# Optimization experiments

Hardware: AMD Instinct MI355X
Metric: run time of the kernel (lower is better)

The kernel has to match this reference:

```python
import jax, jax.numpy as jnp
import numpy as np

B, N, E, S, HOPS, OD = 32, 325, 64, 12, 3, 1


def setup_inputs() -> dict:
    key = jax.random.key(0)
    ks = jax.random.split(key, 16)
    rn = lambda k, sh: jax.random.normal(k, sh, dtype=jnp.float32)
    return {
        "hidden": rn(ks[0], (B, N, E)),
        "supports": jax.random.uniform(ks[1], (2, N, N), dtype=jnp.float32),
        "target": rn(ks[2], (B, S, N, OD)),
        "memory": rn(ks[3], (HOPS + 1, B, N, E)),
        "nodevec1": rn(ks[4], (N, E)),
        "nodevec2": rn(ks[5], (N, E)),
        "gru_w_ih": rn(ks[6], (3 * E, OD)) * 0.1,
        "gru_w_hh": rn(ks[7], (3 * E, E)) * 0.1,
        "gru_b_ih": rn(ks[8], (3 * E,)) * 0.1,
        "gru_b_hh": rn(ks[9], (3 * E,)) * 0.1,
        "sent_w": rn(ks[10], (HOPS, E, E)) * 0.1,  # sentinel Linear (no bias), stored pre-transposed
        "bn_gamma": jnp.ones((HOPS, N), dtype=jnp.float32),
        "bn_beta": jnp.zeros((HOPS, N), dtype=jnp.float32),
        "gconv_w": rn(ks[11], (HOPS, 7 * E, E)) * 0.05,  # order*support_len+1 = 7 chunks
        "gconv_b": rn(ks[12], (HOPS, E)) * 0.05,
        "out_w": rn(ks[13], (E, OD)) * 0.1,
        "out_b": rn(ks[14], (OD,)) * 0.1,
    }


def _bn(x, gamma, beta, eps=1e-5):
    # nn.BatchNorm1d(num_nodes) on (B, N, E): channel dim is N, stats over (B, E) (training-mode batch stats)
    mean = x.mean(axis=(0, 2), keepdims=True)
    var = x.var(axis=(0, 2), keepdims=True)
    return (x - mean) / jnp.sqrt(var + eps) * gamma[None, :, None] + beta[None, :, None]


def _gconv(x, sup_list, score, W, b):
    # order=2, support_len=3 -> 1 + 2*3 = 7 concatenated chunks, then Linear(7E -> E)
    outs = [x]
    for adj in sup_list:
        x1 = jnp.einsum('nm,bme->bne', adj, x)
        outs.append(jnp.einsum('bnm,bme->bne', score, x1))
        x2 = jnp.einsum('nm,bme->bne', adj, x1)
        outs.append(jnp.einsum('bnm,bme->bne', score, x2))
    return jnp.concatenate(outs, axis=-1) @ W + b


def reference(hidden, supports, target, memory, nodevec1, nodevec2,
              gru_w_ih, gru_w_hh, gru_b_ih, gru_b_hh, sent_w,
              bn_gamma, bn_beta, gconv_w, gconv_b, out_w, out_b):
    Bn, Nn, Ee = hidden.shape
    scale = Ee ** 0.5
    adp = jax.nn.softmax(jax.nn.relu(nodevec1 @ nodevec2.T), axis=-1)
    sup_list = [supports[0], supports[1], adp]

    def step(carry, _):
        h, prev = carry  # h: (B,N,E), prev: (B,N,OD) previous prediction (zeros at t=0)
        gi = prev.reshape(Bn * Nn, -1) @ gru_w_ih.T + gru_b_ih
        gh = h.reshape(Bn * Nn, Ee) @ gru_w_hh.T + gru_b_hh
        i_r, i_z, i_n = jnp.split(gi, 3, axis=-1)
        h_r, h_z, h_n = jnp.split(gh, 3, axis=-1)
        r = jax.nn.sigmoid(i_r + h_r)
        z = jax.nn.sigmoid(i_z + h_z)
        n = jnp.tanh(i_n + r * h_n)
        h_new = ((1.0 - z) * n + z * h.reshape(Bn * Nn, Ee)).reshape(Bn, Nn, Ee)
        u = h_new
        sents, mems = [], []
        for hop in range(HOPS):
            key_m = memory[hop]  # (B,N,E)
            energy = jnp.einsum('bne,bme->bnm', u, key_m) / scale  # (B,N,N)
            sent = jnp.sum(u * (key_m @ sent_w[hop]), axis=-1) / scale  # (B,N)
            sents.append(sent)
            score = jax.nn.softmax(energy, axis=-1)
            o = _bn(_gconv(memory[hop + 1], sup_list, score, gconv_w[hop], gconv_b[hop]),
                    bn_gamma[hop], bn_beta[hop])
            mems.append(o)
            u = u + o
        sents = jnp.stack(sents, axis=-1)   # (B,N,hops)
        mems = jnp.stack(mems, axis=-2)     # (B,N,hops,E)
        # NOTE: original code weights with RAW sentinel energies, not sentinel_score (dead code) -- kept faithful
        out = jnp.sum(sents[..., None] * mems, axis=-2) @ out_w + out_b  # (B,N,OD)
        return (h_new, out), out

    init_out = jnp.zeros((Bn, Nn, OD), dtype=hidden.dtype)
    _, outs = jax.lax.scan(step, (hidden, init_out), None, length=S)  # (S,B,N,OD)
    return jnp.transpose(outs, (1, 0, 2, 3))  # (B,S,N,OD)
```

## Files before the change

kernel.cpp:

```cpp
#include <hip/hip_runtime.h>

constexpr int B = 32, N = 325, E = 64, S = 12, HOPS = 3;
constexpr int BN  = B * N;
constexpr int BNE = B * N * E;
constexpr int EP  = E + 4;
constexpr int PBSTR = 360;
constexpr float SCALE_INV = 0.125f;

typedef __attribute__((ext_vector_type(8))) short short8v;
typedef __attribute__((ext_vector_type(4))) float f32x4;

__device__ inline short f2bf(float f) {
  unsigned x = __builtin_bit_cast(unsigned, f);
  return (short)((x + 0x7FFFu + ((x >> 16) & 1u)) >> 16);
}
__device__ inline float bf2f(short h) {
  unsigned x = ((unsigned)(unsigned short)h) << 16;
  return __builtin_bit_cast(float, x);
}

__global__ __launch_bounds__(256) void adp_kernel(const float* __restrict__ nv1,
                                                  const float* __restrict__ nv2,
                                                  float* __restrict__ adp) {
  int n = blockIdx.x;
  __shared__ float row[E];
  __shared__ float buf[N];
  __shared__ float red[256];
  int tid = threadIdx.x;
  if (tid < E) row[tid] = nv1[n * E + tid];
  __syncthreads();
  float lmax = -1e30f;
  for (int m = tid; m < N; m += 256) {
    const float* v2 = nv2 + (size_t)m * E;
    float s = 0.f;
#pragma unroll
    for (int e = 0; e < E; ++e) s += row[e] * v2[e];
    s = fmaxf(s, 0.f);
    buf[m] = s;
    lmax = fmaxf(lmax, s);
  }
  red[tid] = lmax;
  __syncthreads();
  for (int off = 128; off > 0; off >>= 1) {
    if (tid < off) red[tid] = fmaxf(red[tid], red[tid + off]);
    __syncthreads();
  }
  float mx = red[0];
  __syncthreads();
  float lsum = 0.f;
  for (int m = tid; m < N; m += 256) {
    float ev = expf(buf[m] - mx);
    buf[m] = ev;
    lsum += ev;
  }
  red[tid] = lsum;
  __syncthreads();
  for (int off = 128; off > 0; off >>= 1) {
    if (tid < off) red[tid] += red[tid + off];
    __syncthreads();
  }
  float inv = 1.f / red[0];
  for (int m = tid; m < N; m += 256) adp[(size_t)n * N + m] = buf[m] * inv;
}

__device__ inline void rowmm_body(const float* __restrict__ in, const float* __restrict__ W,
                                  const float* __restrict__ bias, float* __restrict__ out,
                                  int accum, int blk, int nblk) {
  __shared__ float Wl[E][E + 1];
  __shared__ float rbuf[4][4][E];
  int tid = threadIdx.x, w = tid >> 6, l = tid & 63;
  for (int idx = tid; idx < E * E; idx += 256) Wl[idx >> 6][idx & 63] = W[idx];
// ... 50 lines not shown
  rowmm_body(tbase + (size_t)h * BNE, gw + (size_t)h * 7 * E * E + (size_t)chunk * E * E,
             nullptr, Zb + (size_t)h * BNE, accum, blk, 224);
}

__global__ __launch_bounds__(64) void apack_kernel(const float* __restrict__ supports,
                                                   const float* __restrict__ adp,
                                                   short* __restrict__ ap) {
  int blk = blockIdx.x;
  int nt = blk % 21, a = blk / 21;
  const float* A = (a < 2) ? supports + (size_t)a * N * N : adp;
  int l = threadIdx.x;
  int row = nt * 16 + (l & 15);
  int k0 = (l >> 4) * 8;
  for (int ks = 0; ks < 11; ++ks) {
    short8v hi, lo;
#pragma unroll
    for (int j = 0; j < 8; ++j) {
      int m = ks * 32 + k0 + j;
      float f = (row < N && m < N) ? A[(size_t)row * N + m] : 0.f;
      short h = f2bf(f);
      hi[j] = h;
      lo[j] = f2bf(f - bf2f(h));
    }
    size_t base = ((size_t)(blk * 11 + ks) * 2) * 512 + (size_t)l * 8;
    *(short8v*)(ap + base) = hi;
    *(short8v*)(ap + base + 512) = lo;
  }
}

__global__ __launch_bounds__(64) void zpack_kernel(const float* __restrict__ Zb,
                                                   short* __restrict__ zp) {
  int idx = blockIdx.x;
  int et = idx & 3, hb = idx >> 2;
  int l = threadIdx.x;
  int e = et * 16 + (l & 15);
  int mbase = (l >> 4) * 8;
  const float* Zp = Zb + (size_t)hb * N * E;
  for (int ks = 0; ks < 11; ++ks) {
    short8v hi, lo;
#pragma unroll
    for (int j = 0; j < 8; ++j) {
      int m = ks * 32 + mbase + j;
      float f = (m < N) ? Zp[(size_t)m * E + e] : 0.f;
      short h = f2bf(f);
      hi[j] = h;
      lo[j] = f2bf(f - bf2f(h));
    }
    size_t base = ((size_t)idx * 11 + ks) * 1024 + (size_t)l * 8;
    *(short8v*)(zp + base) = hi;
    *(short8v*)(zp + base + 512) = lo;
  }
}

__global__ __launch_bounds__(256) void bmmM_kernel(const short* __restrict__ ap,
                                                   const short* __restrict__ xp,
                                                   float* __restrict__ out) {
  int bid = blockIdx.x;
  int x8 = bid & 7, q = bid >> 3;
  int nt = q % 21, hbhi = q / 21;
  int hb = hbhi * 8 + x8;
  int tid = threadIdx.x, w = tid >> 6, l = tid & 63;
  const short8v* apf = (const short8v*)ap;
  const short8v* xpf = (const short8v*)(xp + (((size_t)hb * 4 + w) * 11) * 1024);
  f32x4 acc = {0.f, 0.f, 0.f, 0.f};
#pragma unroll
  for (int ks = 0; ks < 11; ++ks) {
    short8v ah = apf[((nt * 11 + ks) * 2 + 0) * 64 + l];
    short8v al = apf[((nt * 11 + ks) * 2 + 1) * 64 + l];
    short8v xh = xpf[(ks * 2 + 0) * 64 + l];
    short8v xl = xpf[(ks * 2 + 1) * 64 + l];
    acc = __builtin_amdgcn_mfma_f32_16x16x32_bf16(ah, xh, acc, 0, 0, 0);
    acc = __builtin_amdgcn_mfma_f32_16x16x32_bf16(ah, xl, acc, 0, 0, 0);
    acc = __builtin_amdgcn_mfma_f32_16x16x32_bf16(al, xh, acc, 0, 0, 0);
  }
  int row = nt * 16 + (l >> 4) * 4, col = w * 16 + (l & 15);
  float* o = out + (size_t)hb * N * E;
#pragma unroll
  for (int r = 0; r < 4; ++r)
    if (row + r < N) o[(size_t)(row + r) * E + col] = acc[r];
}

__global__ __launch_bounds__(128) void kpack_kernel(const float* __restrict__ memory,
                                                    short* __restrict__ kp) {
  int idx = blockIdx.x;
  int ct = idx % 21, hb = idx / 21;
  int tid = threadIdx.x, ks = tid >> 6, l = tid & 63;
  int m = ct * 16 + (l & 15);
  int e0 = ks * 32 + (l >> 4) * 8;
  short8v hi, lo;
  if (m < N) {
    const float* p = memory + ((size_t)hb * N + m) * E + e0;
#pragma unroll
    for (int j = 0; j < 8; ++j) {
      float f = p[j];
      short h = f2bf(f);
      hi[j] = h;
      lo[j] = f2bf(f - bf2f(h));
    }
  } else {
#pragma unroll
    for (int j = 0; j < 8; ++j) { hi[j] = 0; lo[j] = 0; }
  }
  size_t base = ((size_t)idx * 2 + ks) * 1024 + (size_t)l * 8;
  *(short8v*)(kp + base) = hi;
  *(short8v*)(kp + base + 512) = lo;
}

__global__ __launch_bounds__(512) void attn_kernel(
    const float* __restrict__ uPrev, const float* __restrict__ gprePrev,
    const float* __restrict__ statsPrev, const float* __restrict__ gammaPrev,
    const float* __restrict__ betaPrev, const float* __restrict__ outw,
    float* __restrict__ uOut, float* __restrict__ owPrev,
    const float* __restrict__ kms, const short* __restrict__ kp,
    const short* __restrict__ zp, const float* __restrict__ C0,
    float* __restrict__ gpre, float* __restrict__ statsCur,
    float* __restrict__ sent) {
  int bid = blockIdx.x;
  int x8 = bid & 7, q = bid >> 3;
  int rt = q % 11, bhi = q / 11;
  int b = bhi * 8 + x8;
  int n0 = rt * 32, nrows = min(32, N - n0);
  int tid = threadIdx.x, w = tid >> 6, l = tid & 63;
  __shared__ float uT[32][68];
  __shared__ short pb[32][PBSTR];
  __shared__ float rowred[32][8];
  __shared__ float rmax[32];
  __shared__ float rsinv[32];
  size_t rowbase = (size_t)b * N + n0;
  int g = l >> 4;

  for (int idx = tid; idx < 32 * (PBSTR - 336); idx += 512) {
    int r = idx / (PBSTR - 336), c = idx - r * (PBSTR - 336);
    pb[r][336 + c] = 0;
  }
#pragma unroll
  for (int rr = 0; rr < 4; ++rr) {
    int r = w * 4 + rr;
    if (r < nrows) {
      size_t gi = (rowbase + r) * E + l;
      float uv;
      if (gprePrev) {
        int n = n0 + r;
        float m = statsPrev[n] * (1.f / 2048.f);
        float var = statsPrev[N + n] * (1.f / 2048.f) - m * m;
        float rstd = rsqrtf(var + 1e-5f);
        float o = (gprePrev[gi] - m) * rstd * gammaPrev[n] + betaPrev[n];
        uv = uPrev[gi] + o;
        if (uOut) uOut[gi] = uv;
        float tt = o * outw[l];
#pragma unroll
        for (int off = 32; off; off >>= 1) tt += __shfl_xor(tt, off);
        if (l == 0) owPrev[rowbase + r] = tt;
      } else {
        uv = uPrev[gi];
      }
      uT[r][l] = uv;
    } else {
      uT[r][l] = 0.f;
    }
  }
  __syncthreads();
#pragma unroll
  for (int rr = 0; rr < 4; ++rr) {
    int r = w * 4 + rr;
    if (r < nrows) {
      float v = uT[r][l] * kms[(rowbase + r) * E + l];
#pragma unroll
      for (int off = 32; off; off >>= 1) v += __shfl_xor(v, off);
      if (l == 0) sent[rowbase + r] = v * SCALE_INV;
    }
  }
  short8v ah[2][2], al[2][2];
  {
    int arow = l & 15, ak = g * 8;
#pragma unroll
    for (int mt = 0; mt < 2; ++mt)
#pragma unroll
      for (int ks = 0; ks < 2; ++ks) {
        const float* p = &uT[mt * 16 + arow][ks * 32 + ak];
        short8v h, lo;
#pragma unroll
        for (int j = 0; j < 8; ++j) {
          float f = p[j];
          short hh = f2bf(f);
          h[j] = hh;
          lo[j] = f2bf(f - bf2f(hh));
        }
        ah[mt][ks] = h; al[mt][ks] = lo;
      }
  }
  const short8v* kpb = (const short8v*)(kp + (size_t)b * 21 * 2048);
  f32x4 acc0[3], acc1[3];
#pragma unroll
  for (int i = 0; i < 3; ++i) {
    acc0[i] = (f32x4){0.f, 0.f, 0.f, 0.f};
    acc1[i] = (f32x4){0.f, 0.f, 0.f, 0.f};
    int ct = w + 8 * i;
    if (ct < 21) {
      short8v bh0 = kpb[(ct * 4 + 0) * 64 + l];
      short8v bl0 = kpb[(ct * 4 + 1) * 64 + l];
      short8v bh1 = kpb[(ct * 4 + 2) * 64 + l];
      short8v bl1 = kpb[(ct * 4 + 3) * 64 + l];
      f32x4 a0 = acc0[i], a1 = acc1[i];
      a0 = __builtin_amdgcn_mfma_f32_16x16x32_bf16(ah[0][0], bh0, a0, 0, 0, 0);
      a0 = __builtin_amdgcn_mfma_f32_16x16x32_bf16(ah[0][0], bl0, a0, 0, 0, 0);
      a0 = __builtin_amdgcn_mfma_f32_16x16x32_bf16(al[0][0], bh0, a0, 0, 0, 0);
      a0 = __builtin_amdgcn_mfma_f32_16x16x32_bf16(ah[0][1], bh1, a0, 0, 0, 0);
      a0 = __builtin_amdgcn_mfma_f32_16x16x32_bf16(ah[0][1], bl1, a0, 0, 0, 0);
      a0 = __builtin_amdgcn_mfma_f32_16x16x32_bf16(al[0][1], bh1, a0, 0, 0, 0);
      a1 = __builtin_amdgcn_mfma_f32_16x16x32_bf16(ah[1][0], bh0, a1, 0, 0, 0);
      a1 = __builtin_amdgcn_mfma_f32_16x16x32_bf16(ah[1][0], bl0, a1, 0, 0, 0);
      a1 = __builtin_amdgcn_mfma_f32_16x16x32_bf16(al[1][0], bh0, a1, 0, 0, 0);
      a1 = __builtin_amdgcn_mfma_f32_16x16x32_bf16(ah[1][1], bh1, a1, 0, 0, 0);
      a1 = __builtin_amdgcn_mfma_f32_16x16x32_bf16(ah[1][1], bl1, a1, 0, 0, 0);
      a1 = __builtin_amdgcn_mfma_f32_16x16x32_bf16(al[1][1], bh1, a1, 0, 0, 0);
      acc0[i] = a0; acc1[i] = a1;
    }
  }
  {
    float m0[4], m1[4];
#pragma unroll
    for (int r = 0; r < 4; ++r) {
      float a = -1e30f, c = -1e30f;
#pragma unroll
      for (int i = 0; i < 3; ++i)
        if (w + 8 * i < 21) { a = fmaxf(a, acc0[i][r]); c = fmaxf(c, acc1[i][r]); }
#pragma unroll
      for (int off = 1; off < 16; off <<= 1) {
        a = fmaxf(a, __shfl_xor(a, off));
        c = fmaxf(c, __shfl_xor(c, off));
      }
      m0[r] = a; m1[r] = c;
    }
    if ((l & 15) == 0) {
#pragma unroll
      for (int r = 0; r < 4; ++r) {
        rowred[g * 4 + r][w] = m0[r];
        rowred[16 + g * 4 + r][w] = m1[r];
      }
    }
  }
  __syncthreads();
  if (tid < 32) {
    float a = rowred[tid][0];
#pragma unroll
    for (int j = 1; j < 8; ++j) a = fmaxf(a, rowred[tid][j]);
    rmax[tid] = a;
  }
  __syncthreads();
  {
    float mx0[4], mx1[4], s0[4], s1[4];
#pragma unroll
    for (int r = 0; r < 4; ++r) {
      mx0[r] = rmax[g * 4 + r]; mx1[r] = rmax[16 + g * 4 + r];
      s0[r] = 0.f; s1[r] = 0.f;
    }
#pragma unroll
    for (int i = 0; i < 3; ++i) {
      int ct = w + 8 * i;
      if (ct < 21) {
        int col = ct * 16 + (l & 15);
        bool valid = col < N;
#pragma unroll
        for (int r = 0; r < 4; ++r) {
          short pv0 = 0, pv1 = 0;
          if (valid) {
            pv0 = f2bf(expf((acc0[i][r] - mx0[r]) * SCALE_INV));
            pv1 = f2bf(expf((acc1[i][r] - mx1[r]) * SCALE_INV));
            s0[r] += bf2f(pv0);
            s1[r] += bf2f(pv1);
          }
          pb[g * 4 + r][col] = pv0;
          pb[16 + g * 4 + r][col] = pv1;
        }
      }
    }
#pragma unroll
    for (int r = 0; r < 4; ++r) {
#pragma unroll
      for (int off = 1; off < 16; off <<= 1) {
        s0[r] += __shfl_xor(s0[r], off);
        s1[r] += __shfl_xor(s1[r], off);
      }
    }
    if ((l & 15) == 0) {
#pragma unroll
      for (int r = 0; r < 4; ++r) {
        rowred[g * 4 + r][w] = s0[r];
        rowred[16 + g * 4 + r][w] = s1[r];
      }
    }
  }
  __syncthreads();
  if (tid < 32) {
    float s = 0.f;
#pragma unroll
    for (int j = 0; j < 8; ++j) s += rowred[tid][j];
    rsinv[tid] = 1.f / s;
  }
  __syncthreads();
  int mt = w >> 2, et = w & 3;
  const short8v* zpb = (const short8v*)(zp + (size_t)b * 4 * 11 * 1024);
  f32x4 acc = {0.f, 0.f, 0.f, 0.f};
  {
    int arow = mt * 16 + (l & 15), ak = g * 8;
#pragma unroll
    for (int ks = 0; ks < 11; ++ks) {
      short8v a = *(const short8v*)&pb[arow][ks * 32 + ak];
      short8v zh = zpb[((et * 11 + ks) * 2 + 0) * 64 + l];
      short8v zl = zpb[((et * 11 + ks) * 2 + 1) * 64 + l];
      acc = __builtin_amdgcn_mfma_f32_16x16x32_bf16(a, zh, acc, 0, 0, 0);
      acc = __builtin_amdgcn_mfma_f32_16x16x32_bf16(a, zl, acc, 0, 0, 0);
    }
  }
  int colA = et * 16 + (l & 15);
#pragma unroll
  for (int r = 0; r < 4; ++r) {
    int row = mt * 16 + g * 4 + r;
    float sval = 0.f, qval = 0.f;
    if (row < nrows) {
      size_t gi = (rowbase + row) * E + colA;
      float gA = acc[r] * rsinv[row] + C0[gi];
      gpre[gi] = gA;
      sval = gA; qval = gA * gA;
    }
#pragma unroll
    for (int off = 1; off < 16; off <<= 1) {
      sval += __shfl_xor(sval, off);
      qval += __shfl_xor(qval, off);
    }
    if ((l & 15) == 0 && row < nrows) {
      atomicAdd(&statsCur[n0 + row], sval);
      atomicAdd(&statsCur[N + n0 + row], qval);
    }
  }
}

__global__ __launch_bounds__(256) void gru_kernel(
    float* __restrict__ h,
    const float* __restrict__ gpre2, const float* __restrict__ stats2,
    const float* __restrict__ gamma2, const float* __restrict__ beta2,
    const float* __restrict__ outw, const float* __restrict__ outb,
    const float* __restrict__ sentb, const float* __restrict__ owb,
    float* __restrict__ dout, int tprev,
    const float* __restrict__ wih, const float* __restrict__ whh,
    const float* __restrict__ bih, const float* __restrict__ bhh,
    float* __restrict__ u) {
  __shared__ float W[3 * E][EP];
  __shared__ float hrow[4][E];
  int tid = threadIdx.x, w = tid >> 6, l = tid & 63;
  for (int idx = tid; idx < 3 * E * E; idx += 256) W[idx >> 6][idx & 63] = whh[idx];
  __syncthreads();
  float wi0 = wih[l], wi1 = wih[64 + l], wi2 = wih[128 + l];
  float bi0 = bih[l], bi1 = bih[64 + l], bi2 = bih[128 + l];
  float bh0 = bhh[l], bh1 = bhh[64 + l], bh2 = bhh[128 + l];
  float wv = outw[l];
  float ob = outb[0];
  int nw = gridDim.x * 4, wid = blockIdx.x * 4 + w;
  for (int row = wid; row < BN; row += nw) {
    float hv = h[(size_t)row * E + l];
    hrow[w][l] = hv;
    float pv = 0.f;
    if (gpre2) {
      int n = row % N;
      float m = stats2[n] * (1.f / 2048.f);
      float var = stats2[N + n] * (1.f / 2048.f) - m * m;
      float rstd = rsqrtf(var + 1e-5f);
      float o = (gpre2[(size_t)row * E + l] - m) * rstd * gamma2[n] + beta2[n];
      float tt = o * wv;
#pragma unroll
      for (int off = 32; off; off >>= 1) tt += __shfl_xor(tt, off);
      float v = ob + sentb[row] * owb[row] + sentb[BN + row] * owb[BN + row]
              + sentb[2 * BN + row] * tt;
      pv = v;
      if (l == 0) {
        int bb = row / N;
        dout[((size_t)bb * S + tprev) * N + (row - bb * N)] = v;
      }
    }
    float g0 = bh0, g1 = bh1, g2 = bh2;
#pragma unroll
    for (int k = 0; k < 16; ++k) {
      float4 hh = *(const float4*)&hrow[w][4 * k];
      float4 a = *(const float4*)&W[l][4 * k];
      float4 bq = *(const float4*)&W[64 + l][4 * k];
      float4 c = *(const float4*)&W[128 + l][4 * k];
      g0 += hh.x * a.x + hh.y * a.y + hh.z * a.z + hh.w * a.w;
      g1 += hh.x * bq.x + hh.y * bq.y + hh.z * bq.z + hh.w * bq.w;
      g2 += hh.x * c.x + hh.y * c.y + hh.z * c.z + hh.w * c.w;
    }
    float i0 = pv * wi0 + bi0;
    float i1 = pv * wi1 + bi1;
    float i2 = pv * wi2 + bi2;
    float r = 1.f / (1.f + expf(-(i0 + g0)));
    float z = 1.f / (1.f + expf(-(i1 + g1)));
    float nn = tanhf(i2 + r * g2);
    float hn = (1.f - z) * nn + z * hv;
    h[(size_t)row * E + l] = hn;
    u[(size_t)row * E + l] = hn;
  }
}

__global__ __launch_bounds__(256) void finish_kernel(
    const float* __restrict__ gpre2, const float* __restrict__ stats2,
    const float* __restrict__ gamma2, const float* __restrict__ beta2,
    const float* __restrict__ outw, const float* __restrict__ outb,
    const float* __restrict__ sent, const float* __restrict__ ow01,
    float* __restrict__ dout, int t) {
  int tid = threadIdx.x, w = tid >> 6, l = tid & 63;
  int wid = blockIdx.x * 4 + w, nw = gridDim.x * 4;
  float wv = outw[l];
  for (int row = wid; row < BN; row += nw) {
    int n = row % N;
    float m = stats2[n] * (1.f / 2048.f);
    float var = stats2[N + n] * (1.f / 2048.f) - m * m;
    float rstd = rsqrtf(var + 1e-5f);
    float o = (gpre2[(size_t)row * E + l] - m) * rstd * gamma2[n] + beta2[n];
    float tt = o * wv;
#pragma unroll
    for (int off = 32; off; off >>= 1) tt += __shfl_xor(tt, off);
    if (l == 0) {
      float v = outb[0] + sent[row] * ow01[row] + sent[BN + row] * ow01[BN + row]
              + sent[2 * BN + row] * tt;
      int b = row / N;
      dout[((size_t)b * S + t) * N + (row - b * N)] = v;
    }
  }
}

extern "C" void kernel_launch(void* const* d_in, const int* in_sizes, int n_in,
                              void* d_out, int out_size, void* d_ws, size_t ws_size,
                              hipStream_t stream) {
  const float* hidden   = (const float*)d_in[0];
  const float* supports = (const float*)d_in[1];
  const float* memory   = (const float*)d_in[3];
  const float* nv1      = (const float*)d_in[4];
  const float* nv2      = (const float*)d_in[5];
  const float* wih      = (const float*)d_in[6];
  const float* whh      = (const float*)d_in[7];
  const float* bih      = (const float*)d_in[8];
  const float* bhh      = (const float*)d_in[9];
  const float* sent_w   = (const float*)d_in[10];
  const float* gamma    = (const float*)d_in[11];
  const float* beta     = (const float*)d_in[12];
  const float* gw       = (const float*)d_in[13];
  const float* gb       = (const float*)d_in[14];
  const float* outw     = (const float*)d_in[15];
  const float* outb     = (const float*)d_in[16];
  float* out = (float*)d_out;
  float* ws  = (float*)d_ws;

  size_t o = 0;
  float* adp   = ws + o; o += 105632;
  float* kms   = ws + o; o += (size_t)3 * BNE;
  float* C0b   = ws + o; o += (size_t)3 * BNE;
  float* hbuf  = ws + o; o += (size_t)BNE;
  float* ubuf  = ws + o; o += (size_t)BNE;
  float* u1    = ws + o; o += (size_t)BNE;
  float* uni   = ws + o; o += (size_t)9 * BNE;
  float* Zb  = uni;
  float* t1b = uni + (size_t)3 * BNE;
  float* t2b = uni + (size_t)6 * BNE;
  float* g0 = uni, *g1 = uni + BNE, *g2 = uni + (size_t)2 * BNE;
  short* kpackS = (short*)(ws + o); o += 2064384;
  short* zpackS = (short*)(ws + o); o += 2162688;
  short* apackS = (short*)(ws + o); o += 354816;
  short* xp0    = (short*)(ws + o); o += 2162688;
  short* xp1    = (short*)(ws + o); o += 2162688;
  float* sentb  = ws + o; o += (size_t)3 * BN;
  float* owb    = ws + o; o += (size_t)2 * BN;
  float* statsb = ws + o; o += (size_t)36 * 650;

  hipMemcpyAsync(hbuf, hidden, sizeof(float) * BNE, hipMemcpyDeviceToDevice, stream);
  hipMemsetAsync(statsb, 0, sizeof(float) * 36 * 650, stream);

  adp_kernel<<<N, 256, 0, stream>>>(nv1, nv2, adp);
  rowmmA_kernel<<<672, 256, 0, stream>>>(memory, sent_w, gw, gb, kms, C0b);
  kpack_kernel<<<3 * B * 21, 128, 0, stream>>>(memory, kpackS);
  apack_kernel<<<63, 64, 0, stream>>>(supports, adp, apackS);
  zpack_kernel<<<3 * B * 4, 64, 0, stream>>>(memory + BNE, xp0);

  for (int a = 0; a < 3; ++a) {
    const short* apA = apackS + (size_t)a * 21 * 11 * 2 * 512;
    bmmM_kernel<<<96 * 21, 256, 0, stream>>>(apA, xp0, t1b);
    rowmmZ_kernel<<<672, 256, 0, stream>>>(t1b, gw, 2 * a + 1, Zb, (a > 0) ? 1 : 0);
    zpack_kernel<<<3 * B * 4, 64, 0, stream>>>(t1b, xp1);
    bmmM_kernel<<<96 * 21, 256, 0, stream>>>(apA, xp1, t2b);
    rowmmZ_kernel<<<672, 256, 0, stream>>>(t2b, gw, 2 * a + 2, Zb, 1);
  }
  zpack_kernel<<<3 * B * 4, 64, 0, stream>>>(Zb, zpackS);

  for (int t = 0; t < S; ++t) {
    float* st0 = statsb + (size_t)(t * 3 + 0) * 650;
    float* st1 = statsb + (size_t)(t * 3 + 1) * 650;
    float* st2 = statsb + (size_t)(t * 3 + 2) * 650;
    const float* g2prev  = (t == 0) ? nullptr : g2;
    const float* st2prev = (t == 0) ? nullptr : statsb + (size_t)((t - 1) * 3 + 2) * 650;
    gru_kernel<<<512, 256, 0, stream>>>(hbuf, g2prev, st2prev, gamma + 2 * N, beta + 2 * N,
                                        outw, outb, sentb, owb, out, t - 1,
                                        wih, whh, bih, bhh, ubuf);
    attn_kernel<<<B * 11, 512, 0, stream>>>(
        ubuf, nullptr, nullptr, nullptr, nullptr, outw, nullptr, nullptr,
        kms, kpackS, zpackS, C0b, g0, st0, sentb);
    attn_kernel<<<B * 11, 512, 0, stream>>>(
        ubuf, g0, st0, gamma, beta, outw, u1, owb,
        kms + BNE, kpackS + (size_t)B * 21 * 2048, zpackS + (size_t)B * 4 * 11 * 1024,
        C0b + BNE, g1, st1, sentb + BN);
    attn_kernel<<<B * 11, 512, 0, stream>>>(
        u1, g1, st1, gamma + N, beta + N, outw, nullptr, owb + BN,
        kms + (size_t)2 * BNE, kpackS + (size_t)2 * B * 21 * 2048,
        zpackS + (size_t)2 * B * 4 * 11 * 1024,
        C0b + (size_t)2 * BNE, g2, st2, sentb + (size_t)2 * BN);
  }
  finish_kernel<<<256, 256, 0, stream>>>(g2, statsb + (size_t)(11 * 3 + 2) * 650,
                                         gamma + 2 * N, beta + 2 * N,
                                         outw, outb, sentb, owb, out, S - 1);
}
```

Measured before the change: 2.060 ms.

## Fuse the recurrent GRU and attention hops into one persistent kernel with grid barriers

Replaces the per-timestep launches (a GRU kernel plus three attention kernels per step, then a finish kernel) with a single persistent step_kernel of 352 blocks. A software grid barrier built on atomics handles the cross-block batch-norm statistics dependency. Hidden state, u and gpre now stay in shared memory for each block's 32-row tile instead of round-tripping through global memory. The GRU hidden-to-hidden matmul moves from FP32 shared-memory dot products to split-bf16 MFMA using a packed W_hh. The persistent grid needs every block co-resident, otherwise the barrier deadlocks, and the fused kernel's larger register and shared-memory footprint may lower occupancy.

```diff
diff --git a/kernel.cpp b/kernel.cpp
--- a/kernel.cpp
+++ b/kernel.cpp
@@ -3,8 +3,8 @@
 constexpr int B = 32, N = 325, E = 64, S = 12, HOPS = 3;
 constexpr int BN  = B * N;
 constexpr int BNE = B * N * E;
-constexpr int EP  = E + 4;
 constexpr int PBSTR = 360;
+constexpr int STST = 672;
 constexpr float SCALE_INV = 0.125f;
 
 typedef __attribute__((ext_vector_type(8))) short short8v;
@@ -17,6 +17,26 @@
 __device__ inline float bf2f(short h) {
   unsigned x = ((unsigned)(unsigned short)h) << 16;
   return __builtin_bit_cast(float, x);
+}
+__device__ inline float agent_loadf(const float* p) {
+  return __hip_atomic_load(p, __ATOMIC_RELAXED, __HIP_MEMORY_SCOPE_AGENT);
+}
+
+__device__ inline void grid_barrier(unsigned* bar, unsigned nblk) {
+  __syncthreads();
+  if (threadIdx.x == 0) {
+    __threadfence();
+    unsigned my = __hip_atomic_load(&bar[1], __ATOMIC_ACQUIRE, __HIP_MEMORY_SCOPE_AGENT);
+    unsigned prev = __hip_atomic_fetch_add(&bar[0], 1u, __ATOMIC_ACQ_REL, __HIP_MEMORY_SCOPE_AGENT);
+    if (prev == nblk - 1u) {
+      __hip_atomic_store(&bar[0], 0u, __ATOMIC_RELAXED, __HIP_MEMORY_SCOPE_AGENT);
+      __hip_atomic_fetch_add(&bar[1], 1u, __ATOMIC_RELEASE, __HIP_MEMORY_SCOPE_AGENT);
+    } else {
+      while (__hip_atomic_load(&bar[1], __ATOMIC_ACQUIRE, __HIP_MEMORY_SCOPE_AGENT) == my)
+        __builtin_amdgcn_s_sleep(2);
+    }
+  }
+  __syncthreads();
 }
 
 __global__ __launch_bounds__(256) void adp_kernel(const float* __restrict__ nv1,
@@ -173,6 +193,28 @@
   }
 }
 
+__global__ __launch_bounds__(64) void wpack_kernel(const float* __restrict__ whh,
+                                                   short* __restrict__ wp) {
+  int ot = blockIdx.x;
+  int l = threadIdx.x;
+  int out = ot * 16 + (l & 15);
+  int e0 = (l >> 4) * 8;
+  for (int ks = 0; ks < 2; ++ks) {
+    short8v hi, lo;
+#pragma unroll
+    for (int j = 0; j < 8; ++j) {
+      int e = ks * 32 + e0 + j;
+      float f = whh[(size_t)out * E + e];
+      short h = f2bf(f);
+      hi[j] = h;
+      lo[j] = f2bf(f - bf2f(h));
+    }
+    size_t base = ((size_t)(ot * 2 + ks) * 2) * 512 + (size_t)l * 8;
+    *(short8v*)(wp + base) = hi;
+    *(short8v*)(wp + base + 512) = lo;
+  }
+}
+
 __global__ __launch_bounds__(256) void bmmM_kernel(const short* __restrict__ ap,
                                                    const short* __restrict__ xp,
                                                    float* __restrict__ out) {
@@ -227,324 +269,354 @@
   *(short8v*)(kp + base + 512) = lo;
 }
 
-__global__ __launch_bounds__(512) void attn_kernel(
-    const float* __restrict__ uPrev, const float* __restrict__ gprePrev,
-    const float* __restrict__ statsPrev, const float* __restrict__ gammaPrev,
-    const float* __restrict__ betaPrev, const float* __restrict__ outw,
-    float* __restrict__ uOut, float* __restrict__ owPrev,
-    const float* __restrict__ kms, const short* __restrict__ kp,
-    const short* __restrict__ zp, const float* __restrict__ C0,
-    float* __restrict__ gpre, float* __restrict__ statsCur,
-    float* __restrict__ sent) {
+__global__ __launch_bounds__(512, 4) void step_kernel(
+    const float* __restrict__ hidden,
+    const float* __restrict__ kms,
+    const short* __restrict__ kp,
+    const short* __restrict__ zp,
+    const float* __restrict__ C0,
+    float* __restrict__ statsb,
+    const float* __restrict__ gamma, const float* __restrict__ beta,
+    const float* __restrict__ outw, const float* __restrict__ outb,
+    const float* __restrict__ wih, const short* __restrict__ wp,
+    const float* __restrict__ bih, const float* __restrict__ bhh,
+    unsigned* __restrict__ bar,
+    float* __restrict__ dout) {
+  unsigned nblk = gridDim.x;
   int bid = blockIdx.x;
   int x8 = bid & 7, q = bid >> 3;
   int rt = q % 11, bhi = q / 11;
   int b = bhi * 8 + x8;
   int n0 = rt * 32, nrows = min(32, N - n0);
   int tid = threadIdx.x, w = tid >> 6, l = tid & 63;
+  int g = l >> 4;
+  size_t rowbase = (size_t)b * N + n0;
+
   __shared__ float uT[32][68];
-  __shared__ short pb[32][PBSTR];
+  __shared__ float hT[32][68];
+  __shared__ float gpreL[32][68];
   __shared__ float rowred[32][8];
-  __shared__ float rmax[32];
-  __shared__ float rsinv[32];
-  size_t rowbase = (size_t)b * N + n0;
-  int g = l >> 4;
-
-  for (int idx = tid; idx < 32 * (PBSTR - 336); idx += 512) {
-    int r = idx / (PBSTR - 336), c = idx - r * (PBSTR - 336);
-    pb[r][336 + c] = 0;
-  }
+  __shared__ float rmax[32], rsinv[32];
+  __shared__ float pvL[32], sentL[3][32], owL[2][32];
+  __shared__ __align__(16) char arenaRaw[25600];
+  short (*pb)[PBSTR] = (short (*)[PBSTR])arenaRaw;
+  float (*ghL)[200] = (float (*)[200])arenaRaw;
+
 #pragma unroll
   for (int rr = 0; rr < 4; ++rr) {
     int r = w * 4 + rr;
-    if (r < nrows) {
-      size_t gi = (rowbase + r) * E + l;
-      float uv;
-      if (gprePrev) {
-        int n = n0 + r;
-        float m = statsPrev[n] * (1.f / 2048.f);
-        float var = statsPrev[N + n] * (1.f / 2048.f) - m * m;
-        float rstd = rsqrtf(var + 1e-5f);
-        float o = (gprePrev[gi] - m) * rstd * gammaPrev[n] + betaPrev[n];
-        uv = uPrev[gi] + o;
-        if (uOut) uOut[gi] = uv;
-        float tt = o * outw[l];
-#pragma unroll
-        for (int off = 32; off; off >>= 1) tt += __shfl_xor(tt, off);
-        if (l == 0) owPrev[rowbase + r] = tt;
-      } else {
-        uv = uPrev[gi];
-      }
-      uT[r][l] = uv;
-    } else {
-      uT[r][l] = 0.f;
-    }
-  }
-  __syncthreads();
-#pragma unroll
-  for (int rr = 0; rr < 4; ++rr) {
-    int r = w * 4 + rr;
-    if (r < nrows) {
-      float v = uT[r][l] * kms[(rowbase + r) * E + l];
-#pragma unroll
-      for (int off = 32; off; off >>= 1) v += __shfl_xor(v, off);
-      if (l == 0) sent[rowbase + r] = v * SCALE_INV;
-    }
-  }
-  short8v ah[2][2], al[2][2];
-  {
-    int arow = l & 15, ak = g * 8;
-#pragma unroll
-    for (int mt = 0; mt < 2; ++mt)
-#pragma unroll
-      for (int ks = 0; ks < 2; ++ks) {
-        const float* p = &uT[mt * 16 + arow][ks * 32 + ak];
-        short8v h, lo;
-#pragma unroll
-        for (int j = 0; j < 8; ++j) {
-          float f = p[j];
-          short hh = f2bf(f);
-          h[j] = hh;
-          lo[j] = f2bf(f - bf2f(hh));
-        }
-        ah[mt][ks] = h; al[mt][ks] = lo;
-      }
-  }
-  const short8v* kpb = (const short8v*)(kp + (size_t)b * 21 * 2048);
-  f32x4 acc0[3], acc1[3];
-#pragma unroll
-  for (int i = 0; i < 3; ++i) {
-    acc0[i] = (f32x4){0.f, 0.f, 0.f, 0.f};
-    acc1[i] = (f32x4){0.f, 0.f, 0.f, 0.f};
-    int ct = w + 8 * i;
-    if (ct < 21) {
-      short8v bh0 = kpb[(ct * 4 + 0) * 64 + l];
-      short8v bl0 = kpb[(ct * 4 + 1) * 64 + l];
-      short8v bh1 = kpb[(ct * 4 + 2) * 64 + l];
-      short8v bl1 = kpb[(ct * 4 + 3) * 64 + l];
-      f32x4 a0 = acc0[i], a1 = acc1[i];
-      a0 = __builtin_amdgcn_mfma_f32_16x16x32_bf16(ah[0][0], bh0, a0, 0, 0, 0);
-      a0 = __builtin_amdgcn_mfma_f32_16x16x32_bf16(ah[0][0], bl0, a0, 0, 0, 0);
-      a0 = __builtin_amdgcn_mfma_f32_16x16x32_bf16(al[0][0], bh0, a0, 0, 0, 0);
-      a0 = __builtin_amdgcn_mfma_f32_16x16x32_bf16(ah[0][1], bh1, a0, 0, 0, 0);
-      a0 = __builtin_amdgcn_mfma_f32_16x16x32_bf16(ah[0][1], bl1, a0, 0, 0, 0);
-      a0 = __builtin_amdgcn_mfma_f32_16x16x32_bf16(al[0][1], bh1, a0, 0, 0, 0);
-      a1 = __builtin_amdgcn_mfma_f32_16x16x32_bf16(ah[1][0], bh0, a1, 0, 0, 0);
-      a1 = __builtin_amdgcn_mfma_f32_16x16x32_bf16(ah[1][0], bl0, a1, 0, 0, 0);
-      a1 = __builtin_amdgcn_mfma_f32_16x16x32_bf16(al[1][0], bh0, a1, 0, 0, 0);
-      a1 = __builtin_amdgcn_mfma_f32_16x16x32_bf16(ah[1][1], bh1, a1, 0, 0, 0);
-      a1 = __builtin_amdgcn_mfma_f32_16x16x32_bf16(ah[1][1], bl1, a1, 0, 0, 0);
-      a1 = __builtin_amdgcn_mfma_f32_16x16x32_bf16(al[1][1], bh1, a1, 0, 0, 0);
-      acc0[i] = a0; acc1[i] = a1;
-    }
-  }
-  {
-    float m0[4], m1[4];
-#pragma unroll
-    for (int r = 0; r < 4; ++r) {
-      float a = -1e30f, c = -1e30f;
-#pragma unroll
-      for (int i = 0; i < 3; ++i)
-        if (w + 8 * i < 21) { a = fmaxf(a, acc0[i][r]); c = fmaxf(c, acc1[i][r]); }
-#pragma unroll
-      for (int off = 1; off < 16; off <<= 1) {
-        a = fmaxf(a, __shfl_xor(a, off));
-        c = fmaxf(c, __shfl_xor(c, off));
-      }
-      m0[r] = a; m1[r] = c;
-    }
-    if ((l & 15) == 0) {
-#pragma unroll
-      for (int r = 0; r < 4; ++r) {
-        rowred[g * 4 + r][w] = m0[r];
-        rowred[16 + g * 4 + r][w] = m1[r];
-      }
-    }
-  }
-  __syncthreads();
-  if (tid < 32) {
-    float a = rowred[tid][0];
-#pragma unroll
-    for (int j = 1; j < 8; ++j) a = fmaxf(a, rowred[tid][j]);
-    rmax[tid] = a;
-  }
-  __syncthreads();
-  {
-    float mx0[4], mx1[4], s0[4], s1[4];
-#pragma unroll
-    for (int r = 0; r < 4; ++r) {
-      mx0[r] = rmax[g * 4 + r]; mx1[r] = rmax[16 + g * 4 + r];
-      s0[r] = 0.f; s1[r] = 0.f;
-    }
-#pragma unroll
-    for (int i = 0; i < 3; ++i) {
-      int ct = w + 8 * i;
-      if (ct < 21) {
-        int col = ct * 16 + (l & 15);
-        bool valid = col < N;
-#pragma unroll
-        for (int r = 0; r < 4; ++r) {
-          short pv0 = 0, pv1 = 0;
-          if (valid) {
-            pv0 = f2bf(expf((acc0[i][r] - mx0[r]) * SCALE_INV));
-            pv1 = f2bf(expf((acc1[i][r] - mx1[r]) * SCALE_INV));
-            s0[r] += bf2f(pv0);
-            s1[r] += bf2f(pv1);
-          }
-          pb[g * 4 + r][col] = pv0;
-          pb[16 + g * 4 + r][col] = pv1;
-        }
-      }
-    }
-#pragma unroll
-    for (int r = 0; r < 4; ++r) {
-#pragma unroll
-      for (int off = 1; off < 16; off <<= 1) {
-        s0[r] += __shfl_xor(s0[r], off);
-        s1[r] += __shfl_xor(s1[r], off);
-      }
-    }
-    if ((l & 15) == 0) {
-#pragma unroll
-      for (int r = 0; r < 4; ++r) {
-        rowred[g * 4 + r][w] = s0[r];
-        rowred[16 + g * 4 + r][w] = s1[r];
-      }
-    }
-  }
-  __syncthreads();
-  if (tid < 32) {
-    float s = 0.f;
-#pragma unroll
-    for (int j = 0; j < 8; ++j) s += rowred[tid][j];
-    rsinv[tid] = 1.f / s;
-  }
-  __syncthreads();
-  int mt = w >> 2, et = w & 3;
-  const short8v* zpb = (const short8v*)(zp + (size_t)b * 4 * 11 * 1024);
-  f32x4 acc = {0.f, 0.f, 0.f, 0.f};
-  {
-    int arow = mt * 16 + (l & 15), ak = g * 8;
-#pragma unroll
-    for (int ks = 0; ks < 11; ++ks) {
-      short8v a = *(const short8v*)&pb[arow][ks * 32 + ak];
-      short8v zh = zpb[((et * 11 + ks) * 2 + 0) * 64 + l];
-      short8v zl = zpb[((et * 11 + ks) * 2 + 1) * 64 + l];
-      acc = __builtin_amdgcn_mfma_f32_16x16x32_bf16(a, zh, acc, 0, 0, 0);
-      acc = __builtin_amdgcn_mfma_f32_16x16x32_bf16(a, zl, acc, 0, 0, 0);
-    }
-  }
-  int colA = et * 16 + (l & 15);
-#pragma unroll
-  for (int r = 0; r < 4; ++r) {
-    int row = mt * 16 + g * 4 + r;
-    float sval = 0.f, qval = 0.f;
-    if (row < nrows) {
-      size_t gi = (rowbase + row) * E + colA;
-      float gA = acc[r] * rsinv[row] + C0[gi];
-      gpre[gi] = gA;
-      sval = gA; qval = gA * gA;
-    }
-#pragma unroll
-    for (int off = 1; off < 16; off <<= 1) {
-      sval += __shfl_xor(sval, off);
-      qval += __shfl_xor(qval, off);
-    }
-    if ((l & 15) == 0 && row < nrows) {
-      atomicAdd(&statsCur[n0 + row], sval);
-      atomicAdd(&statsCur[N + n0 + row], qval);
-    }
-  }
-}
-
-__global__ __launch_bounds__(256) void gru_kernel(
-    float* __restrict__ h,
-    const float* __restrict__ gpre2, const float* __restrict__ stats2,
-    const float* __restrict__ gamma2, const float* __restrict__ beta2,
-    const float* __restrict__ outw, const float* __restrict__ outb,
-    const float* __restrict__ sentb, const float* __restrict__ owb,
-    float* __restrict__ dout, int tprev,
-    const float* __restrict__ wih, const float* __restrict__ whh,
-    const float* __restrict__ bih, const float* __restrict__ bhh,
-    float* __restrict__ u) {
-  __shared__ float W[3 * E][EP];
-  __shared__ float hrow[4][E];
-  int tid = threadIdx.x, w = tid >> 6, l = tid & 63;
-  for (int idx = tid; idx < 3 * E * E; idx += 256) W[idx >> 6][idx & 63] = whh[idx];
-  __syncthreads();
+    hT[r][l] = (r < nrows) ? hidden[(rowbase + r) * E + l] : 0.f;
+    if (l == 0) pvL[r] = 0.f;
+  }
   float wi0 = wih[l], wi1 = wih[64 + l], wi2 = wih[128 + l];
   float bi0 = bih[l], bi1 = bih[64 + l], bi2 = bih[128 + l];
   float bh0 = bhh[l], bh1 = bhh[64 + l], bh2 = bhh[128 + l];
-  float wv = outw[l];
+  float owv = outw[l];
   float ob = outb[0];
-  int nw = gridDim.x * 4, wid = blockIdx.x * 4 + w;
-  for (int row = wid; row < BN; row += nw) {
-    float hv = h[(size_t)row * E + l];
-    hrow[w][l] = hv;
-    float pv = 0.f;
-    if (gpre2) {
-      int n = row % N;
-      float m = stats2[n] * (1.f / 2048.f);
-      float var = stats2[N + n] * (1.f / 2048.f) - m * m;
-      float rstd = rsqrtf(var + 1e-5f);
-      float o = (gpre2[(size_t)row * E + l] - m) * rstd * gamma2[n] + beta2[n];
-      float tt = o * wv;
-#pragma unroll
-      for (int off = 32; off; off >>= 1) tt += __shfl_xor(tt, off);
-      float v = ob + sentb[row] * owb[row] + sentb[BN + row] * owb[BN + row]
-              + sentb[2 * BN + row] * tt;
-      pv = v;
-      if (l == 0) {
-        int bb = row / N;
-        dout[((size_t)bb * S + tprev) * N + (row - bb * N)] = v;
-      }
-    }
-    float g0 = bh0, g1 = bh1, g2 = bh2;
-#pragma unroll
-    for (int k = 0; k < 16; ++k) {
-      float4 hh = *(const float4*)&hrow[w][4 * k];
-      float4 a = *(const float4*)&W[l][4 * k];
-      float4 bq = *(const float4*)&W[64 + l][4 * k];
-      float4 c = *(const float4*)&W[128 + l][4 * k];
-      g0 += hh.x * a.x + hh.y * a.y + hh.z * a.z + hh.w * a.w;
-      g1 += hh.x * bq.x + hh.y * bq.y + hh.z * bq.z + hh.w * bq.w;
-      g2 += hh.x * c.x + hh.y * c.y + hh.z * c.z + hh.w * c.w;
-    }
-    float i0 = pv * wi0 + bi0;
-    float i1 = pv * wi1 + bi1;
-    float i2 = pv * wi2 + bi2;
-    float r = 1.f / (1.f + expf(-(i0 + g0)));
-    float z = 1.f / (1.f + expf(-(i1 + g1)));
-    float nn = tanhf(i2 + r * g2);
-    float hn = (1.f - z) * nn + z * hv;
-    h[(size_t)row * E + l] = hn;
-    u[(size_t)row * E + l] = hn;
-  }
-}
-
-__global__ __launch_bounds__(256) void finish_kernel(
-    const float* __restrict__ gpre2, const float* __restrict__ stats2,
-    const float* __restrict__ gamma2, const float* __restrict__ beta2,
-    const float* __restrict__ outw, const float* __restrict__ outb,
-    const float* __restrict__ sent, const float* __restrict__ ow01,
-    float* __restrict__ dout, int t) {
-  int tid = threadIdx.x, w = tid >> 6, l = tid & 63;
-  int wid = blockIdx.x * 4 + w, nw = gridDim.x * 4;
-  float wv = outw[l];
-  for (int row = wid; row < BN; row += nw) {
-    int n = row % N;
-    float m = stats2[n] * (1.f / 2048.f);
-    float var = stats2[N + n] * (1.f / 2048.f) - m * m;
-    float rstd = rsqrtf(var + 1e-5f);
-    float o = (gpre2[(size_t)row * E + l] - m) * rstd * gamma2[n] + beta2[n];
-    float tt = o * wv;
-#pragma unroll
-    for (int off = 32; off; off >>= 1) tt += __shfl_xor(tt, off);
-    if (l == 0) {
-      float v = outb[0] + sent[row] * ow01[row] + sent[BN + row] * ow01[BN + row]
-              + sent[2 * BN + row] * tt;
-      int b = row / N;
-      dout[((size_t)b * S + t) * N + (row - b * N)] = v;
+  __syncthreads();
+
+  for (int t = 0; t < S; ++t) {
+    if (t > 0) {
+      const float* st2 = statsb + (size_t)((t - 1) * 3 + 2) * STST;
+#pragma unroll
+      for (int rr = 0; rr < 4; ++rr) {
+        int r = w * 4 + rr, n = n0 + r;
+        if (r < nrows) {
+          float m = agent_loadf(&st2[n]) * (1.f / 2048.f);
+          float var = agent_loadf(&st2[N + n]) * (1.f / 2048.f) - m * m;
+          float rstd = rsqrtf(var + 1e-5f);
+          float o = (gpreL[r][l] - m) * rstd * gamma[2 * N + n] + beta[2 * N + n];
+          float tt = o * owv;
+#pragma unroll
+          for (int off = 32; off; off >>= 1) tt += __shfl_xor(tt, off);
+          float v = ob + sentL[0][r] * owL[0][r] + sentL[1][r] * owL[1][r] + sentL[2][r] * tt;
+          if (l == 0) {
+            dout[((size_t)b * S + (t - 1)) * N + n] = v;
+            pvL[r] = v;
+          }
+        }
+      }
+      __syncthreads();
+    }
+    short8v hah[2][2], hal[2][2];
+    {
+      int arow = l & 15, ak = g * 8;
+#pragma unroll
+      for (int mt = 0; mt < 2; ++mt)
+#pragma unroll
+        for (int ks = 0; ks < 2; ++ks) {
+          const float* p = &hT[mt * 16 + arow][ks * 32 + ak];
+          short8v h, lo;
+#pragma unroll
+          for (int j = 0; j < 8; ++j) {
+            float f = p[j];
+            short hh = f2bf(f);
+            h[j] = hh;
+            lo[j] = f2bf(f - bf2f(hh));
+          }
+          hah[mt][ks] = h; hal[mt][ks] = lo;
+        }
+    }
+    const short8v* wpf = (const short8v*)wp;
+#pragma unroll
+    for (int i = 0; i < 3; ++i) {
+      int idx = w * 3 + i;
+      int mt = idx / 12, ot = idx % 12;
+      f32x4 acc = {0.f, 0.f, 0.f, 0.f};
+#pragma unroll
+      for (int ks = 0; ks < 2; ++ks) {
+        short8v wh = wpf[((ot * 2 + ks) * 2 + 0) * 64 + l];
+        short8v wl = wpf[((ot * 2 + ks) * 2 + 1) * 64 + l];
+        acc = __builtin_amdgcn_mfma_f32_16x16x32_bf16(hah[mt][ks], wh, acc, 0, 0, 0);
+        acc = __builtin_amdgcn_mfma_f32_16x16x32_bf16(hah[mt][ks], wl, acc, 0, 0, 0);
+        acc = __builtin_amdgcn_mfma_f32_16x16x32_bf16(hal[mt][ks], wh, acc, 0, 0, 0);
+      }
+      int row0 = mt * 16 + g * 4, col = ot * 16 + (l & 15);
+#pragma unroll
+      for (int r = 0; r < 4; ++r) ghL[row0 + r][col] = acc[r];
+    }
+    __syncthreads();
+#pragma unroll
+    for (int rr = 0; rr < 4; ++rr) {
+      int r = w * 4 + rr;
+      float hv = hT[r][l];
+      float g0 = ghL[r][l] + bh0;
+      float g1 = ghL[r][64 + l] + bh1;
+      float g2 = ghL[r][128 + l] + bh2;
+      float pv = pvL[r];
+      float i0 = pv * wi0 + bi0, i1 = pv * wi1 + bi1, i2 = pv * wi2 + bi2;
+      float rg = 1.f / (1.f + expf(-(i0 + g0)));
+      float zg = 1.f / (1.f + expf(-(i1 + g1)));
+      float nn = tanhf(i2 + rg * g2);
+      float hn = (1.f - zg) * nn + zg * hv;
+      if (r >= nrows) hn = 0.f;
+      hT[r][l] = hn;
+      uT[r][l] = hn;
+    }
+    __syncthreads();
+    for (int idx2 = tid; idx2 < 32 * (PBSTR - 336); idx2 += 512) {
+      int r = idx2 / (PBSTR - 336), c = idx2 - r * (PBSTR - 336);
+      pb[r][336 + c] = 0;
+    }
+    __syncthreads();
+    for (int h = 0; h < 3; ++h) {
+      if (h > 0) {
+        const float* stp = statsb + (size_t)(t * 3 + h - 1) * STST;
+        const float* gm = gamma + (h - 1) * N;
+        const float* bt = beta + (h - 1) * N;
+#pragma unroll
+        for (int rr = 0; rr < 4; ++rr) {
+          int r = w * 4 + rr, n = n0 + r;
+          if (r < nrows) {
+            float m = agent_loadf(&stp[n]) * (1.f / 2048.f);
+            float var = agent_loadf(&stp[N + n]) * (1.f / 2048.f) - m * m;
+            float rstd = rsqrtf(var + 1e-5f);
+            float o = (gpreL[r][l] - m) * rstd * gm[n] + bt[n];
+            uT[r][l] += o;
+            float tt = o * owv;
+#pragma unroll
+            for (int off = 32; off; off >>= 1) tt += __shfl_xor(tt, off);
+            if (l == 0) owL[h - 1][r] = tt;
+          }
+        }
+        __syncthreads();
+      }
+      const float* kmsH = kms + (size_t)h * BNE;
+#pragma unroll
+      for (int rr = 0; rr < 4; ++rr) {
+        int r = w * 4 + rr;
+        if (r < nrows) {
+          float v = uT[r][l] * kmsH[(rowbase + r) * E + l];
+#pragma unroll
+          for (int off = 32; off; off >>= 1) v += __shfl_xor(v, off);
+          if (l == 0) sentL[h][r] = v * SCALE_INV;
+        }
+      }
+      short8v ah[2][2], al[2][2];
+      {
+        int arow = l & 15, ak = g * 8;
+#pragma unroll
+        for (int mt = 0; mt < 2; ++mt)
+#pragma unroll
+          for (int ks = 0; ks < 2; ++ks) {
+            const float* p = &uT[mt * 16 + arow][ks * 32 + ak];
+            short8v hh_, lo_;
+#pragma unroll
+            for (int j = 0; j < 8; ++j) {
+              float f = p[j];
+              short hh = f2bf(f);
+              hh_[j] = hh;
+              lo_[j] = f2bf(f - bf2f(hh));
+            }
+            ah[mt][ks] = hh_; al[mt][ks] = lo_;
+          }
+      }
+      const short8v* kpb = (const short8v*)(kp + ((size_t)h * B + b) * 21 * 2048);
+      f32x4 acc0[3], acc1[3];
+#pragma unroll
+      for (int i = 0; i < 3; ++i) {
+        acc0[i] = (f32x4){0.f, 0.f, 0.f, 0.f};
+        acc1[i] = (f32x4){0.f, 0.f, 0.f, 0.f};
+        int ct = w + 8 * i;
+        if (ct < 21) {
+          short8v bh0v = kpb[(ct * 4 + 0) * 64 + l];
+          short8v bl0v = kpb[(ct * 4 + 1) * 64 + l];
+          short8v bh1v = kpb[(ct * 4 + 2) * 64 + l];
+          short8v bl1v = kpb[(ct * 4 + 3) * 64 + l];
+          f32x4 a0 = acc0[i], a1 = acc1[i];
+          a0 = __builtin_amdgcn_mfma_f32_16x16x32_bf16(ah[0][0], bh0v, a0, 0, 0, 0);
+          a0 = __builtin_amdgcn_mfma_f32_16x16x32_bf16(ah[0][0], bl0v, a0, 0, 0, 0);
+          a0 = __builtin_amdgcn_mfma_f32_16x16x32_bf16(al[0][0], bh0v, a0, 0, 0, 0);
+          a0 = __builtin_amdgcn_mfma_f32_16x16x32_bf16(ah[0][1], bh1v, a0, 0, 0, 0);
+          a0 = __builtin_amdgcn_mfma_f32_16x16x32_bf16(ah[0][1], bl1v, a0, 0, 0, 0);
+          a0 = __builtin_amdgcn_mfma_f32_16x16x32_bf16(al[0][1], bh1v, a0, 0, 0, 0);
+          a1 = __builtin_amdgcn_mfma_f32_16x16x32_bf16(ah[1][0], bh0v, a1, 0, 0, 0);
+          a1 = __builtin_amdgcn_mfma_f32_16x16x32_bf16(ah[1][0], bl0v, a1, 0, 0, 0);
+          a1 = __builtin_amdgcn_mfma_f32_16x16x32_bf16(al[1][0], bh0v, a1, 0, 0, 0);
+          a1 = __builtin_amdgcn_mfma_f32_16x16x32_bf16(ah[1][1], bh1v, a1, 0, 0, 0);
+          a1 = __builtin_amdgcn_mfma_f32_16x16x32_bf16(ah[1][1], bl1v, a1, 0, 0, 0);
+          a1 = __builtin_amdgcn_mfma_f32_16x16x32_bf16(al[1][1], bh1v, a1, 0, 0, 0);
+          acc0[i] = a0; acc1[i] = a1;
+        }
+      }
+      {
+        float m0[4], m1[4];
+#pragma unroll
+        for (int r = 0; r < 4; ++r) {
+          float a = -1e30f, c = -1e30f;
+#pragma unroll
+          for (int i = 0; i < 3; ++i)
+            if (w + 8 * i < 21) { a = fmaxf(a, acc0[i][r]); c = fmaxf(c, acc1[i][r]); }
+#pragma unroll
+          for (int off = 1; off < 16; off <<= 1) {
+            a = fmaxf(a, __shfl_xor(a, off));
+            c = fmaxf(c, __shfl_xor(c, off));
+          }
+          m0[r] = a; m1[r] = c;
+        }
+        if ((l & 15) == 0) {
+#pragma unroll
+          for (int r = 0; r < 4; ++r) {
+            rowred[g * 4 + r][w] = m0[r];
+            rowred[16 + g * 4 + r][w] = m1[r];
+          }
+        }
+      }
+      __syncthreads();
+      if (tid < 32) {
+        float a = rowred[tid][0];
+#pragma unroll
+        for (int j = 1; j < 8; ++j) a = fmaxf(a, rowred[tid][j]);
+        rmax[tid] = a;
+      }
+      __syncthreads();
+      {
+        float mx0[4], mx1[4], s0[4], s1[4];
+#pragma unroll
+        for (int r = 0; r < 4; ++r) {
+          mx0[r] = rmax[g * 4 + r]; mx1[r] = rmax[16 + g * 4 + r];
+          s0[r] = 0.f; s1[r] = 0.f;
+        }
+#pragma unroll
+        for (int i = 0; i < 3; ++i) {
+          int ct = w + 8 * i;
+          if (ct < 21) {
+            int col = ct * 16 + (l & 15);
+            bool valid = col < N;
+#pragma unroll
+            for (int r = 0; r < 4; ++r) {
+              short pv0 = 0, pv1 = 0;
+              if (valid) {
+                pv0 = f2bf(expf((acc0[i][r] - mx0[r]) * SCALE_INV));
+                pv1 = f2bf(expf((acc1[i][r] - mx1[r]) * SCALE_INV));
+                s0[r] += bf2f(pv0);
+                s1[r] += bf2f(pv1);
+              }
+              pb[g * 4 + r][col] = pv0;
+              pb[16 + g * 4 + r][col] = pv1;
+            }
+          }
+        }
+#pragma unroll
+        for (int r = 0; r < 4; ++r) {
+#pragma unroll
+          for (int off = 1; off < 16; off <<= 1) {
+            s0[r] += __shfl_xor(s0[r], off);
+            s1[r] += __shfl_xor(s1[r], off);
+          }
+        }
+        if ((l & 15) == 0) {
+#pragma unroll
+          for (int r = 0; r < 4; ++r) {
+            rowred[g * 4 + r][w] = s0[r];
+            rowred[16 + g * 4 + r][w] = s1[r];
+          }
+        }
+      }
+      __syncthreads();
+      if (tid < 32) {
+        float s = 0.f;
+#pragma unroll
+        for (int j = 0; j < 8; ++j) s += rowred[tid][j];
+        rsinv[tid] = 1.f / s;
+      }
+      __syncthreads();
+      int mt2 = w >> 2, et = w & 3;
+      const short8v* zpb = (const short8v*)(zp + ((size_t)h * B + b) * 4 * 11 * 1024);
+      f32x4 acc = {0.f, 0.f, 0.f, 0.f};
+      {
+        int arow = mt2 * 16 + (l & 15), ak = g * 8;
+#pragma unroll
+        for (int ks = 0; ks < 11; ++ks) {
+          short8v a = *(const short8v*)&pb[arow][ks * 32 + ak];
+          short8v zh = zpb[((et * 11 + ks) * 2 + 0) * 64 + l];
+          short8v zl = zpb[((et * 11 + ks) * 2 + 1) * 64 + l];
+          acc = __builtin_amdgcn_mfma_f32_16x16x32_bf16(a, zh, acc, 0, 0, 0);
+          acc = __builtin_amdgcn_mfma_f32_16x16x32_bf16(a, zl, acc, 0, 0, 0);
+        }
+      }
+      const float* C0h = C0 + (size_t)h * BNE;
+      float* stc = statsb + (size_t)(t * 3 + h) * STST;
+      int colA = et * 16 + (l & 15);
+#pragma unroll
+      for (int r = 0; r < 4; ++r) {
+        int row = mt2 * 16 + g * 4 + r;
+        float sval = 0.f, qval = 0.f;
+        if (row < nrows) {
+          size_t gi = (rowbase + row) * E + colA;
+          float gA = acc[r] * rsinv[row] + C0h[gi];
+          gpreL[row][colA] = gA;
+          sval = gA; qval = gA * gA;
+        }
+#pragma unroll
+        for (int off = 1; off < 16; off <<= 1) {
+          sval += __shfl_xor(sval, off);
+          qval += __shfl_xor(qval, off);
+        }
+        if ((l & 15) == 0 && row < nrows) {
+          atomicAdd(&stc[n0 + row], sval);
+          atomicAdd(&stc[N + n0 + row], qval);
+        }
+      }
+      grid_barrier(bar, nblk);
+    }
+  }
+  {
+    const float* st2 = statsb + (size_t)((S - 1) * 3 + 2) * STST;
+#pragma unroll
+    for (int rr = 0; rr < 4; ++rr) {
+      int r = w * 4 + rr, n = n0 + r;
+      if (r < nrows) {
+        float m = agent_loadf(&st2[n]) * (1.f / 2048.f);
+        float var = agent_loadf(&st2[N + n]) * (1.f / 2048.f) - m * m;
+        float rstd = rsqrtf(var + 1e-5f);
+        float o = (gpreL[r][l] - m) * rstd * gamma[2 * N + n] + beta[2 * N + n];
+        float tt = o * owv;
+#pragma unroll
+        for (int off = 32; off; off >>= 1) tt += __shfl_xor(tt, off);
+        float v = ob + sentL[0][r] * owL[0][r] + sentL[1][r] * owL[1][r] + sentL[2][r] * tt;
+        if (l == 0) dout[((size_t)b * S + (S - 1)) * N + n] = v;
+      }
     }
   }
 }
@@ -575,30 +647,27 @@
   float* adp   = ws + o; o += 105632;
   float* kms   = ws + o; o += (size_t)3 * BNE;
   float* C0b   = ws + o; o += (size_t)3 * BNE;
-  float* hbuf  = ws + o; o += (size_t)BNE;
-  float* ubuf  = ws + o; o += (size_t)BNE;
-  float* u1    = ws + o; o += (size_t)BNE;
   float* uni   = ws + o; o += (size_t)9 * BNE;
   float* Zb  = uni;
   float* t1b = uni + (size_t)3 * BNE;
   float* t2b = uni + (size_t)6 * BNE;
-  float* g0 = uni, *g1 = uni + BNE, *g2 = uni + (size_t)2 * BNE;
   short* kpackS = (short*)(ws + o); o += 2064384;
   short* zpackS = (short*)(ws + o); o += 2162688;
   short* apackS = (short*)(ws + o); o += 354816;
+  short* wpackS = (short*)(ws + o); o += 12288;
   short* xp0    = (short*)(ws + o); o += 2162688;
   short* xp1    = (short*)(ws + o); o += 2162688;
-  float* sentb  = ws + o; o += (size_t)3 * BN;
-  float* owb    = ws + o; o += (size_t)2 * BN;
-  float* statsb = ws + o; o += (size_t)36 * 650;
-
-  hipMemcpyAsync(hbuf, hidden, sizeof(float) * BNE, hipMemcpyDeviceToDevice, stream);
-  hipMemsetAsync(statsb, 0, sizeof(float) * 36 * 650, stream);
+  float* statsb = ws + o; o += (size_t)36 * STST;
+  unsigned* bar = (unsigned*)(ws + o); o += 64;
+
+  hipMemsetAsync(statsb, 0, sizeof(float) * 36 * STST, stream);
+  hipMemsetAsync(bar, 0, sizeof(unsigned) * 64, stream);
 
   adp_kernel<<<N, 256, 0, stream>>>(nv1, nv2, adp);
   rowmmA_kernel<<<672, 256, 0, stream>>>(memory, sent_w, gw, gb, kms, C0b);
   kpack_kernel<<<3 * B * 21, 128, 0, stream>>>(memory, kpackS);
   apack_kernel<<<63, 64, 0, stream>>>(supports, adp, apackS);
+  wpack_kernel<<<12, 64, 0, stream>>>(whh, wpackS);
   zpack_kernel<<<3 * B * 4, 64, 0, stream>>>(memory + BNE, xp0);
 
   for (int a = 0; a < 3; ++a) {
@@ -611,29 +680,7 @@
   }
   zpack_kernel<<<3 * B * 4, 64, 0, stream>>>(Zb, zpackS);
 
-  for (int t = 0; t < S; ++t) {
-    float* st0 = statsb + (size_t)(t * 3 + 0) * 650;
-    float* st1 = statsb + (size_t)(t * 3 + 1) * 650;
-    float* st2 = statsb + (size_t)(t * 3 + 2) * 650;
-    const float* g2prev  = (t == 0) ? nullptr : g2;
-    const float* st2prev = (t == 0) ? nullptr : statsb + (size_t)((t - 1) * 3 + 2) * 650;
-    gru_kernel<<<512, 256, 0, stream>>>(hbuf, g2prev, st2prev, gamma + 2 * N, beta + 2 * N,
-                                        outw, outb, sentb, owb, out, t - 1,
-                                        wih, whh, bih, bhh, ubuf);
-    attn_kernel<<<B * 11, 512, 0, stream>>>(
-        ubuf, nullptr, nullptr, nullptr, nullptr, outw, nullptr, nullptr,
-        kms, kpackS, zpackS, C0b, g0, st0, sentb);
-    attn_kernel<<<B * 11, 512, 0, stream>>>(
-        ubuf, g0, st0, gamma, beta, outw, u1, owb,
-        kms + BNE, kpackS + (size_t)B * 21 * 2048, zpackS + (size_t)B * 4 * 11 * 1024,
-        C0b + BNE, g1, st1, sentb + BN);
-    attn_kernel<<<B * 11, 512, 0, stream>>>(
-        u1, g1, st1, gamma + N, beta + N, outw, nullptr, owb + BN,
-        kms + (size_t)2 * BNE, kpackS + (size_t)2 * B * 21 * 2048,
-        zpackS + (size_t)2 * B * 4 * 11 * 1024,
-        C0b + (size_t)2 * BNE, g2, st2, sentb + (size_t)2 * BN);
-  }
-  finish_kernel<<<256, 256, 0, stream>>>(g2, statsb + (size_t)(11 * 3 + 2) * 650,
-                                         gamma + 2 * N, beta + 2 * N,
-                                         outw, outb, sentb, owb, out, S - 1);
-}
+  step_kernel<<<B * 11, 512, 0, stream>>>(hidden, kms, kpackS, zpackS, C0b, statsb,
+                                          gamma, beta, outw, outb, wih, wpackS,
+                                          bih, bhh, bar, out);
+}
```

Result: slower. 6.089 ms (+195.5%).
